# Optimization experiments

Hardware: AMD Instinct MI355X
Metric: run time of the kernel (lower is better)

Reference implementation:

```python
import jax, jax.numpy as jnp
import numpy as np

B, S, D, H = 2, 2048, 1024, 16
DK = D // H  # 64


def setup_inputs() -> dict:
    key = jax.random.key(0)
    ks = jax.random.split(key, 11)
    std = 1.0 / np.sqrt(D)
    inp = {
        "q": jax.random.normal(ks[0], (B, S, D), jnp.float32),
        "k": jax.random.normal(ks[1], (B, S, D), jnp.float32),
        "v": jax.random.normal(ks[2], (B, S, D), jnp.float32),
        # causal mask: True means masked (matches masked_fill(mask == True, -1e9))
        "mask": jnp.triu(jnp.ones((1, 1, S, S), dtype=bool), k=1),
        "Wq": jax.random.normal(ks[3], (D, D), jnp.float32) * std,
        "bq": jnp.zeros((D,), jnp.float32),
        "Wk": jax.random.normal(ks[4], (D, D), jnp.float32) * std,
        "bk": jnp.zeros((D,), jnp.float32),
        "Wv": jax.random.normal(ks[5], (D, D), jnp.float32) * std,
        "bv": jnp.zeros((D,), jnp.float32),
        "Wo": jax.random.normal(ks[6], (D, D), jnp.float32) * std,
        "bo": jnp.zeros((D,), jnp.float32),
    }
    return inp


def _split_heads(x):
    b, s, _ = x.shape
    return x.reshape(b, s, H, DK).transpose(0, 2, 1, 3)  # [B,H,S,DK]


def reference(q, k, v, mask, Wq, bq, Wk, bk, Wv, bv, Wo, bo):
    # QKV projections (nn.Linear: x @ W.T + b)
    qh = _split_heads(q @ Wq.T + bq)
    kh = _split_heads(k @ Wk.T + bk)
    vh = _split_heads(v @ Wv.T + bv)
    # scaled dot-product attention (dropout is identity in eval)
    scores = jnp.einsum("bhqd,bhkd->bhqk", qh, kh) / jnp.sqrt(
        jnp.asarray(DK, jnp.float32))
    scores = jnp.where(mask, jnp.float32(-1e9), scores)
    attn = jax.nn.softmax(scores, axis=-1)
    out = jnp.einsum("bhqk,bhkd->bhqd", attn, vh)
    # combine heads [B,H,S,DK] -> [B,S,D], then output projection
    out = out.transpose(0, 2, 1, 3).reshape(q.shape[0], -1, D)
    return out @ Wo.T + bo
```

## Files before the change

kernel.cpp:

```cpp
#include <hip/hip_runtime.h>
#include <stdint.h>

#define S_LEN 2048
#define DMODEL 1024
#define NHEAD 16
#define DKH 64

typedef __attribute__((ext_vector_type(8))) short short8;
typedef __attribute__((ext_vector_type(4))) short sv4;
typedef __attribute__((ext_vector_type(4))) float fv4;
typedef __attribute__((ext_vector_type(8))) __bf16 bf16x8;
typedef __attribute__((ext_vector_type(4))) float f32x4;

#define QSCALE 0.18033688011112042f

static __device__ __forceinline__ short f2bf(float f) {
  unsigned u = __builtin_bit_cast(unsigned, f);
  u = u + 0x7fffu + ((u >> 16) & 1u);
  return (short)(u >> 16);
}

static __device__ __forceinline__ bf16x8 ldfrag(const void* p) {
  return __builtin_bit_cast(bf16x8, *(const short8*)p);
}

#define GLL16(gp, lp) __builtin_amdgcn_global_load_lds( \
    (const __attribute__((address_space(1))) unsigned int*)(const void*)(gp), \
    (__attribute__((address_space(3))) unsigned int*)(void*)(lp), 16, 0, 0)

#define WAIT_VMCNT(N) asm volatile("s_waitcnt vmcnt(" #N ")" ::: "memory")
#define WAIT_LGKM0()  asm volatile("s_waitcnt lgkmcnt(0)" ::: "memory")

__global__ __launch_bounds__(256) void convert_all(
    const float* __restrict__ q, const float* __restrict__ k, const float* __restrict__ v,
    const float* __restrict__ wq, const float* __restrict__ wk, const float* __restrict__ wv,
    const float* __restrict__ wo,
    short* __restrict__ xb, short* __restrict__ wb, short* __restrict__ wob)
{
  const int total = 4194304;
  for (int gid = blockIdx.x * blockDim.x + threadIdx.x; gid < total;
       gid += gridDim.x * blockDim.x) {
    const float* src; short* dst; int off; float scl = 1.0f;
    if (gid < 3145728) {
      int z = gid >> 20;
      off = (gid & 1048575) << 2;
      src = (z == 0) ? q : (z == 1) ? k : v;
      dst = xb + (size_t)z * 4194304;
    } else {
      int g = gid - 3145728;
      int z = g >> 18;
      off = (g & 262143) << 2;
      src = (z == 0) ? wq : (z == 1) ? wk : (z == 2) ? wv : wo;
      dst = (z < 3) ? (wb + (size_t)z * 1048576) : wob;
      if (z == 0) scl = QSCALE;
    }
    fv4 f = *(const fv4*)(src + off);
    sv4 o;
    o.x = f2bf(f.x * scl); o.y = f2bf(f.y * scl);
    o.z = f2bf(f.z * scl); o.w = f2bf(f.w * scl);
    *(sv4*)(dst + off) = o;
  }
}

__global__ __launch_bounds__(256) void gemm_proj(
    const short* __restrict__ Abase, const short* __restrict__ Wbase,
    const float* __restrict__ bias0, const float* __restrict__ bias1,
    const float* __restrict__ bias2, float bscl0,
    short* __restrict__ Cbf)
{
  const int Kd = 1024, Nd = 1024, Md = 4096;
  const int z = blockIdx.z;
  const short* A = Abase + (size_t)z * Md * Kd;
  const short* W = Wbase + (size_t)z * Nd * Kd;
  const float* bias = (z == 0) ? bias0 : (z == 1) ? bias1 : bias2;
  const float bscl = (z == 0) ? bscl0 : 1.0f;

  __shared__ short8 AB[4096];

  const int tid = threadIdx.x;
  const int w = tid >> 6, lane = tid & 63;
  const int wr = w >> 1, wc = w & 1;
  const int lhi = lane >> 4, llo = lane & 15;
  const int id = blockIdx.x + 8 * blockIdx.y;
  const int sw = (id & 7) * 32 + (id >> 3);
  const int n0 = (sw & 7) * 128, m0 = (sw >> 3) * 128;

  const f32x4 zero = {0.f, 0.f, 0.f, 0.f};
  f32x4 acc[4][4];
#pragma unroll
  for (int i = 0; i < 4; ++i)
#pragma unroll
    for (int j = 0; j < 4; ++j) acc[i][j] = zero;

  auto stage = [&](int buf, int k0) {
#pragma unroll
    for (int inst = 0; inst < 4; ++inst) {
      int ib = w * 4096 + inst * 1024 + lane * 16;
      int row = ib >> 7;
      int colb = (ib & 127) ^ ((row & 7) << 4);
      int col = colb >> 1;
      GLL16(A + (size_t)(m0 + row) * Kd + k0 + col,
            (char*)AB + buf * 32768 + (w * 4096 + inst * 1024));
      GLL16(W + (size_t)(n0 + row) * Kd + k0 + col,
            (char*)AB + buf * 32768 + 16384 + (w * 4096 + inst * 1024));
    }
  };

  stage(0, 0);
  for (int kt = 0; kt < 16; ++kt) {
    const int cur = kt & 1, nxt = cur ^ 1;
    if (kt < 15) {
      stage(nxt, (kt + 1) * 64);
      WAIT_VMCNT(8);
    } else {
      WAIT_VMCNT(0);
    }
    __builtin_amdgcn_s_barrier();
    const char* As = (const char*)AB + cur * 32768;
    const char* Bs = As + 16384;
#pragma unroll
    for (int kk = 0; kk < 2; ++kk) {
      bf16x8 af[4], bfm[4];
#pragma unroll
      for (int t = 0; t < 4; ++t) {
        int arow = wr * 64 + t * 16 + llo;
        int abyte = ((arow << 7) + ((kk * 32 + lhi * 8) << 1)) ^ ((arow & 7) << 4);
        af[t] = ldfrag(As + abyte);
        int brow = wc * 64 + t * 16 + llo;
        int bbyte = ((brow << 7) + ((kk * 32 + lhi * 8) << 1)) ^ ((brow & 7) << 4);
        bfm[t] = ldfrag(Bs + bbyte);
      }
#pragma unroll
      for (int i = 0; i < 4; ++i)
#pragma unroll
        for (int j = 0; j < 4; ++j)
          acc[i][j] = __builtin_amdgcn_mfma_f32_16x16x32_bf16(af[i], bfm[j], acc[i][j], 0, 0, 0);
    }
    __builtin_amdgcn_s_barrier();
  }

  short* Co = Cbf + (size_t)z * Md * Nd;
  __syncthreads();
  short* Cs = (short*)AB;
#pragma unroll
  for (int i = 0; i < 4; ++i) {
#pragma unroll
    for (int j = 0; j < 4; ++j) {
      int col = wc * 64 + j * 16 + llo;
      float bv_ = bias[n0 + col] * bscl;
#pragma unroll
      for (int r = 0; r < 4; ++r) {
        int row = wr * 64 + i * 16 + lhi * 4 + r;
        Cs[row * 128 + col] = f2bf(acc[i][j][r] + bv_);
      }
    }
  }
  __syncthreads();
#pragma unroll
  for (int s = 0; s < 8; ++s) {
    int lb = s * 4096 + tid * 16;
    short8 vL = *(const short8*)((const char*)Cs + lb);
    int row = lb >> 8;
    int colb = lb & 255;
    *(short8*)&Co[(size_t)(m0 + row) * Nd + n0 + (colb >> 1)] = vL;
  }
}

__global__ __launch_bounds__(256) void gemm_out(
    const short* __restrict__ A, const short* __restrict__ W,
    const float* __restrict__ bias, float* __restrict__ Cf)
{
  const int Kd = 1024, Nd = 1024;

  __shared__ short8 AB[3072];

  const int tid = threadIdx.x;
  const int w = tid >> 6, lane = tid & 63;
  const int wr = w >> 1, wc = w & 1;
  const int lhi = lane >> 4, llo = lane & 15;
  const int id = blockIdx.x + 16 * blockIdx.y;
  const int sw = (id & 7) * 64 + (id >> 3);
  const int n0 = (sw & 15) * 64, m0 = (sw >> 4) * 128;

  const f32x4 zero = {0.f, 0.f, 0.f, 0.f};
  f32x4 acc[4][2];
#pragma unroll
  for (int i = 0; i < 4; ++i)
#pragma unroll
    for (int j = 0; j < 2; ++j) acc[i][j] = zero;

  auto stage = [&](int buf, int k0) {
#pragma unroll
    for (int inst = 0; inst < 4; ++inst) {
      int ib = w * 4096 + inst * 1024 + lane * 16;
      int row = ib >> 7;
      int colb = (ib & 127) ^ ((row & 7) << 4);
      GLL16(A + (size_t)(m0 + row) * Kd + k0 + (colb >> 1),
            (char*)AB + buf * 24576 + (w * 4096 + inst * 1024));
    }
#pragma unroll
    for (int inst = 0; inst < 2; ++inst) {
      int ib = w * 2048 + inst * 1024 + lane * 16;
      int row = ib >> 7;
      int colb = (ib & 127) ^ ((row & 7) << 4);
      GLL16(W + (size_t)(n0 + row) * Kd + k0 + (colb >> 1),
            (char*)AB + buf * 24576 + 16384 + (w * 2048 + inst * 1024));
    }
  };

  stage(0, 0);
  for (int kt = 0; kt < 16; ++kt) {
    const int cur = kt & 1, nxt = cur ^ 1;
    if (kt < 15) {
      stage(nxt, (kt + 1) * 64);
      WAIT_VMCNT(6);
    } else {
      WAIT_VMCNT(0);
    }
    __builtin_amdgcn_s_barrier();
    const char* As = (const char*)AB + cur * 24576;
    const char* Bs = As + 16384;
#pragma unroll
    for (int kk = 0; kk < 2; ++kk) {
      bf16x8 af[4], bfm[2];
#pragma unroll
      for (int t = 0; t < 4; ++t) {
        int arow = wr * 64 + t * 16 + llo;
        int abyte = ((arow << 7) + ((kk * 32 + lhi * 8) << 1)) ^ ((arow & 7) << 4);
        af[t] = ldfrag(As + abyte);
      }
#pragma unroll
      for (int j = 0; j < 2; ++j) {
        int brow = wc * 32 + j * 16 + llo;
        int bbyte = ((brow << 7) + ((kk * 32 + lhi * 8) << 1)) ^ ((brow & 7) << 4);
        bfm[j] = ldfrag(Bs + bbyte);
      }
#pragma unroll
      for (int i = 0; i < 4; ++i)
#pragma unroll
        for (int j = 0; j < 2; ++j)
          acc[i][j] = __builtin_amdgcn_mfma_f32_16x16x32_bf16(af[i], bfm[j], acc[i][j], 0, 0, 0);
    }
    __builtin_amdgcn_s_barrier();
  }

#pragma unroll
  for (int i = 0; i < 4; ++i) {
#pragma unroll
    for (int j = 0; j < 2; ++j) {
      int col = n0 + wc * 32 + j * 16 + llo;
      float bv_ = bias[col];
#pragma unroll
      for (int r = 0; r < 4; ++r) {
        int row = m0 + wr * 64 + i * 16 + lhi * 4 + r;
        Cf[(size_t)row * Nd + col] = acc[i][j][r] + bv_;
      }
    }
  }
}

__global__ __launch_bounds__(512) void attn_fwd(
    const short* __restrict__ Qp, const short* __restrict__ Kp,
    const short* __restrict__ Vp, short* __restrict__ Out)
{
  __shared__ short8 Ks[2][512];
  __shared__ short  Vt[64 * 72];
  __shared__ short  PsA[8][16 * 72];

  const int tid = threadIdx.x;
  const int w = tid >> 6, lane = tid & 63;
  const int lhi = lane >> 4, llo = lane & 15;

  const int id = blockIdx.x;
  const int half = id >> 8;
  const int g = id & 255;
  const int bh = g >> 3;
  const int wv = g & 7;
  const int qt = half ? (15 - 2 * wv) : (2 * wv);
  const int nt = 2 * qt + 2;
  const int qbase = qt * 128;
  const int b = bh >> 4, h = bh & 15;
  const size_t rowbase = (size_t)b * S_LEN;
  const short* Kbase = Kp + rowbase * DMODEL + h * DKH;
  const short* Vbase = Vp + rowbase * DMODEL + h * DKH;

  short* Ps = PsA[w];
  const f32x4 zero = {0.f, 0.f, 0.f, 0.f};

  bf16x8 qf[2];
  {
    const short* qrow = Qp + (rowbase + qbase + w * 16 + llo) * DMODEL + h * DKH;
    qf[0] = ldfrag(qrow + lhi * 8);
    qf[1] = ldfrag(qrow + 32 + lhi * 8);
  }

  float mr[4], lr[4];
  f32x4 oacc[4];
#pragma unroll
  for (int r = 0; r < 4; ++r) { mr[r] = -3.0e38f; lr[r] = 0.f; }
#pragma unroll
  for (int dt = 0; dt < 4; ++dt) oacc[dt] = zero;

  const int kvs = lane;

  {
    int ib = tid * 16;
    int row = ib >> 7;
    int colb = (ib & 127) ^ ((row & 7) << 4);
    GLL16(Kbase + (size_t)row * DMODEL + (colb >> 1), (char*)&Ks[0][0] + ib);
  }
  short8 va = *(const short8*)(Vbase + (size_t)kvs * DMODEL + w * 8);

  for (int t = 0; t < nt; ++t) {
    const int cur = t & 1, nxt = cur ^ 1;
    const int kvbase = t * 64;

    asm volatile("s_waitcnt vmcnt(0)" ::: "memory");
#pragma unroll
    for (int j = 0; j < 8; ++j) Vt[(w * 8 + j) * 72 + kvs] = va[j];
    if (t + 1 < nt) {
      const int nb = kvbase + 64;
      int ib = tid * 16;
      int row = ib >> 7;
      int colb = (ib & 127) ^ ((row & 7) << 4);
      GLL16(Kbase + (size_t)(nb + row) * DMODEL + (colb >> 1),
            (char*)&Ks[nxt][0] + ib);
      va = *(const short8*)(Vbase + (size_t)(nb + kvs) * DMODEL + w * 8);
    }
    WAIT_LGKM0();
    __builtin_amdgcn_s_barrier();

    f32x4 sc[4];
#pragma unroll
    for (int tt = 0; tt < 4; ++tt) sc[tt] = zero;
    __builtin_amdgcn_s_setprio(1);
#pragma unroll
    for (int kk = 0; kk < 2; ++kk) {
#pragma unroll
      for (int tt = 0; tt < 4; ++tt) {
        int krow = tt * 16 + llo;
        int kbyte = ((krow << 7) + ((kk * 32 + lhi * 8) << 1)) ^ ((krow & 7) << 4);
        bf16x8 kf = ldfrag((const char*)&Ks[cur][0] + kbyte);
        sc[tt] = __builtin_amdgcn_mfma_f32_16x16x32_bf16(qf[kk], kf, sc[tt], 0, 0, 0);
      }
    }
    __builtin_amdgcn_s_setprio(0);

    const bool diag = (t >= nt - 2);
    float sv[4][4], tmx[4];
#pragma unroll
    for (int r = 0; r < 4; ++r) {
#pragma unroll
      for (int tt = 0; tt < 4; ++tt) {
        float s = sc[tt][r];
        if (diag) {
          int kg = kvbase + tt * 16 + llo;
          int qg = qbase + w * 16 + lhi * 4 + r;
          if (kg > qg) s = -3.0e38f;
        }
        sv[tt][r] = s;
      }
      float trm = fmaxf(fmaxf(sv[0][r], sv[1][r]), fmaxf(sv[2][r], sv[3][r]));
      trm = fmaxf(trm, __shfl_xor(trm, 1));
      trm = fmaxf(trm, __shfl_xor(trm, 2));
      trm = fmaxf(trm, __shfl_xor(trm, 4));
      trm = fmaxf(trm, __shfl_xor(trm, 8));
      tmx[r] = trm;
    }
    bool grow = (tmx[0] > mr[0] + 8.f) || (tmx[1] > mr[1] + 8.f) ||
                (tmx[2] > mr[2] + 8.f) || (tmx[3] > mr[3] + 8.f);
    if (__ballot(grow)) {
#pragma unroll
      for (int r = 0; r < 4; ++r) {
        float mnew = fmaxf(mr[r], tmx[r]);
        float alpha = __builtin_amdgcn_exp2f(mr[r] - mnew);
        mr[r] = mnew;
        lr[r] *= alpha;
#pragma unroll
        for (int dt = 0; dt < 4; ++dt) oacc[dt][r] = oacc[dt][r] * alpha;
      }
    }
#pragma unroll
    for (int r = 0; r < 4; ++r) {
      float rs = 0.f;
#pragma unroll
      for (int tt = 0; tt < 4; ++tt) {
        float pv = __builtin_amdgcn_exp2f(sv[tt][r] - mr[r]);
        rs += pv;
        Ps[(lhi * 4 + r) * 72 + tt * 16 + llo] = f2bf(pv);
      }
      lr[r] += rs;
    }

    __builtin_amdgcn_s_setprio(1);
#pragma unroll
    for (int kk = 0; kk < 2; ++kk) {
      bf16x8 pa = ldfrag(Ps + llo * 72 + kk * 32 + lhi * 8);
#pragma unroll
      for (int dt = 0; dt < 4; ++dt) {
        bf16x8 vf = ldfrag(&Vt[(dt * 16 + llo) * 72 + kk * 32 + lhi * 8]);
        oacc[dt] = __builtin_amdgcn_mfma_f32_16x16x32_bf16(pa, vf, oacc[dt], 0, 0, 0);
      }
    }
    __builtin_amdgcn_s_setprio(0);
    __builtin_amdgcn_s_barrier();
  }

#pragma unroll
  for (int r = 0; r < 4; ++r) {
    float rs = lr[r];
    rs += __shfl_xor(rs, 1);
    rs += __shfl_xor(rs, 2);
    rs += __shfl_xor(rs, 4);
    rs += __shfl_xor(rs, 8);
    lr[r] = rs;
  }
#pragma unroll
  for (int dt = 0; dt < 4; ++dt) {
#pragma unroll
    for (int r = 0; r < 4; ++r) {
      float vv = oacc[dt][r] / lr[r];
      int row = qbase + w * 16 + lhi * 4 + r;
      int col = h * DKH + dt * 16 + llo;
      Out[(rowbase + row) * DMODEL + col] = f2bf(vv);
    }
  }
}

extern "C" void kernel_launch(void* const* d_in, const int* in_sizes, int n_in,
                              void* d_out, int out_size, void* d_ws, size_t ws_size,
                              hipStream_t stream) {
  (void)in_sizes; (void)n_in; (void)out_size; (void)ws_size;
  const float* q  = (const float*)d_in[0];
  const float* k  = (const float*)d_in[1];
  const float* v  = (const float*)d_in[2];
  const float* Wq = (const float*)d_in[4];
  const float* bq = (const float*)d_in[5];
  const float* Wk = (const float*)d_in[6];
  const float* bk = (const float*)d_in[7];
  const float* Wv = (const float*)d_in[8];
  const float* bv = (const float*)d_in[9];
  const float* Wo = (const float*)d_in[10];
  const float* bo = (const float*)d_in[11];
  float* out = (float*)d_out;

  short* xb   = (short*)d_ws;
  short* wb   = xb + 3ull * 4194304;
  short* wob  = wb + 3ull * 1048576;
  short* proj = wob + 1048576;
  short* attno = xb;

  convert_all<<<dim3(2048), dim3(256), 0, stream>>>(q, k, v, Wq, Wk, Wv, Wo, xb, wb, wob);
  gemm_proj<<<dim3(8, 32, 3), dim3(256), 0, stream>>>(xb, wb, bq, bk, bv, QSCALE, proj);
  attn_fwd<<<dim3(512), dim3(512), 0, stream>>>(proj, proj + 4194304ull,
                                                proj + 2ull * 4194304, attno);
  gemm_out<<<dim3(16, 32), dim3(256), 0, stream>>>(attno, wob, bo, out);
}
```

Baseline: 257.3 us.

## Transpose attention MFMAs and keep P in registers with smaller query tiles

The attention kernel now computes S^T and O^T by swapping the MFMA operands, so each lane owns one query row. P probabilities are packed with v_cvt_pk_bf16_f32 and redistributed through lane shuffles instead of a shared-memory round trip, and the per-row max and sum reductions shrink to two cross-lane steps. Query tiles drop from 128 to 64 rows with 256-thread blocks and 1024 blocks, balanced across four causal groupings. This aims to remove LDS traffic and reductions for P and to improve load balance, at the cost of extra shuffles and reloading K/V more often per query row.

```diff
diff --git a/kernel.cpp b/kernel.cpp
--- a/kernel.cpp
+++ b/kernel.cpp
@@ -11,6 +11,8 @@
 typedef __attribute__((ext_vector_type(4))) float fv4;
 typedef __attribute__((ext_vector_type(8))) __bf16 bf16x8;
 typedef __attribute__((ext_vector_type(4))) float f32x4;
+typedef __attribute__((ext_vector_type(2))) unsigned int u32x2;
+typedef __attribute__((ext_vector_type(4))) unsigned int u32x4;
 
 #define QSCALE 0.18033688011112042f
 
@@ -18,6 +20,12 @@
   unsigned u = __builtin_bit_cast(unsigned, f);
   u = u + 0x7fffu + ((u >> 16) & 1u);
   return (short)(u >> 16);
+}
+
+static __device__ __forceinline__ unsigned cvtpk(float a, float b) {
+  unsigned r;
+  asm("v_cvt_pk_bf16_f32 %0, %1, %2" : "=v"(r) : "v"(a), "v"(b));
+  return r;
 }
 
 static __device__ __forceinline__ bf16x8 ldfrag(const void* p) {
@@ -259,32 +267,31 @@
   }
 }
 
-__global__ __launch_bounds__(512) void attn_fwd(
+__global__ __launch_bounds__(256) void attn_fwd(
     const short* __restrict__ Qp, const short* __restrict__ Kp,
     const short* __restrict__ Vp, short* __restrict__ Out)
 {
   __shared__ short8 Ks[2][512];
   __shared__ short  Vt[64 * 72];
-  __shared__ short  PsA[8][16 * 72];
 
   const int tid = threadIdx.x;
   const int w = tid >> 6, lane = tid & 63;
   const int lhi = lane >> 4, llo = lane & 15;
 
   const int id = blockIdx.x;
-  const int half = id >> 8;
-  const int g = id & 255;
+  const int g  = id & 255;
+  const int kq = id >> 8;
+  const int wv = g & 7;
   const int bh = g >> 3;
-  const int wv = g & 7;
-  const int qt = half ? (15 - 2 * wv) : (2 * wv);
-  const int nt = 2 * qt + 2;
-  const int qbase = qt * 128;
+  const int qt = (kq == 0) ? 2 * wv : (kq == 1) ? 31 - 2 * wv
+               : (kq == 2) ? 2 * wv + 1 : 30 - 2 * wv;
+  const int nt = qt + 1;
+  const int qbase = qt * 64;
   const int b = bh >> 4, h = bh & 15;
   const size_t rowbase = (size_t)b * S_LEN;
   const short* Kbase = Kp + rowbase * DMODEL + h * DKH;
   const short* Vbase = Vp + rowbase * DMODEL + h * DKH;
 
-  short* Ps = PsA[w];
   const f32x4 zero = {0.f, 0.f, 0.f, 0.f};
 
   bf16x8 qf[2];
@@ -294,38 +301,50 @@
     qf[1] = ldfrag(qrow + 32 + lhi * 8);
   }
 
-  float mr[4], lr[4];
+  float mr = -3.0e38f, lr = 0.f;
   f32x4 oacc[4];
 #pragma unroll
-  for (int r = 0; r < 4; ++r) { mr[r] = -3.0e38f; lr[r] = 0.f; }
-#pragma unroll
   for (int dt = 0; dt < 4; ++dt) oacc[dt] = zero;
 
-  const int kvs = lane;
-
-  {
-    int ib = tid * 16;
+  const int kvs = lane, dgrp = w;
+
+  const int srcA = (2 * (lhi & 1)) * 16 + llo;
+  const int srcB = srcA + 16;
+  const int t0d = lhi >> 1;
+
+#pragma unroll
+  for (int inst = 0; inst < 2; ++inst) {
+    int ib = w * 2048 + inst * 1024 + lane * 16;
     int row = ib >> 7;
     int colb = (ib & 127) ^ ((row & 7) << 4);
-    GLL16(Kbase + (size_t)row * DMODEL + (colb >> 1), (char*)&Ks[0][0] + ib);
-  }
-  short8 va = *(const short8*)(Vbase + (size_t)kvs * DMODEL + w * 8);
+    GLL16(Kbase + (size_t)row * DMODEL + (colb >> 1),
+          (char*)&Ks[0][0] + (w * 2048 + inst * 1024));
+  }
+  short8 va, vb;
+  va = *(const short8*)(Vbase + (size_t)kvs * DMODEL + dgrp * 16);
+  vb = *(const short8*)(Vbase + (size_t)kvs * DMODEL + dgrp * 16 + 8);
 
   for (int t = 0; t < nt; ++t) {
     const int cur = t & 1, nxt = cur ^ 1;
     const int kvbase = t * 64;
 
-    asm volatile("s_waitcnt vmcnt(0)" ::: "memory");
-#pragma unroll
-    for (int j = 0; j < 8; ++j) Vt[(w * 8 + j) * 72 + kvs] = va[j];
+    WAIT_VMCNT(0);
+#pragma unroll
+    for (int j = 0; j < 8; ++j) Vt[(dgrp * 16 + j) * 72 + kvs] = va[j];
+#pragma unroll
+    for (int j = 0; j < 8; ++j) Vt[(dgrp * 16 + 8 + j) * 72 + kvs] = vb[j];
     if (t + 1 < nt) {
       const int nb = kvbase + 64;
-      int ib = tid * 16;
-      int row = ib >> 7;
-      int colb = (ib & 127) ^ ((row & 7) << 4);
-      GLL16(Kbase + (size_t)(nb + row) * DMODEL + (colb >> 1),
-            (char*)&Ks[nxt][0] + ib);
-      va = *(const short8*)(Vbase + (size_t)(nb + kvs) * DMODEL + w * 8);
+#pragma unroll
+      for (int inst = 0; inst < 2; ++inst) {
+        int ib = w * 2048 + inst * 1024 + lane * 16;
+        int row = ib >> 7;
+        int colb = (ib & 127) ^ ((row & 7) << 4);
+        GLL16(Kbase + (size_t)(nb + row) * DMODEL + (colb >> 1),
+              (char*)&Ks[nxt][0] + (w * 2048 + inst * 1024));
+      }
+      va = *(const short8*)(Vbase + (size_t)(nb + kvs) * DMODEL + dgrp * 16);
+      vb = *(const short8*)(Vbase + (size_t)(nb + kvs) * DMODEL + dgrp * 16 + 8);
     }
     WAIT_LGKM0();
     __builtin_amdgcn_s_barrier();
@@ -341,88 +360,96 @@
         int krow = tt * 16 + llo;
         int kbyte = ((krow << 7) + ((kk * 32 + lhi * 8) << 1)) ^ ((krow & 7) << 4);
         bf16x8 kf = ldfrag((const char*)&Ks[cur][0] + kbyte);
-        sc[tt] = __builtin_amdgcn_mfma_f32_16x16x32_bf16(qf[kk], kf, sc[tt], 0, 0, 0);
+        sc[tt] = __builtin_amdgcn_mfma_f32_16x16x32_bf16(kf, qf[kk], sc[tt], 0, 0, 0);
       }
     }
     __builtin_amdgcn_s_setprio(0);
 
-    const bool diag = (t >= nt - 2);
-    float sv[4][4], tmx[4];
-#pragma unroll
-    for (int r = 0; r < 4; ++r) {
-#pragma unroll
-      for (int tt = 0; tt < 4; ++tt) {
+    const bool diag = (t == qt);
+    float sv[4][4];
+#pragma unroll
+    for (int tt = 0; tt < 4; ++tt) {
+#pragma unroll
+      for (int r = 0; r < 4; ++r) {
         float s = sc[tt][r];
         if (diag) {
-          int kg = kvbase + tt * 16 + llo;
-          int qg = qbase + w * 16 + lhi * 4 + r;
+          int kg = kvbase + tt * 16 + lhi * 4 + r;
+          int qg = qbase + w * 16 + llo;
           if (kg > qg) s = -3.0e38f;
         }
         sv[tt][r] = s;
       }
-      float trm = fmaxf(fmaxf(sv[0][r], sv[1][r]), fmaxf(sv[2][r], sv[3][r]));
-      trm = fmaxf(trm, __shfl_xor(trm, 1));
-      trm = fmaxf(trm, __shfl_xor(trm, 2));
-      trm = fmaxf(trm, __shfl_xor(trm, 4));
-      trm = fmaxf(trm, __shfl_xor(trm, 8));
-      tmx[r] = trm;
-    }
-    bool grow = (tmx[0] > mr[0] + 8.f) || (tmx[1] > mr[1] + 8.f) ||
-                (tmx[2] > mr[2] + 8.f) || (tmx[3] > mr[3] + 8.f);
-    if (__ballot(grow)) {
+    }
+    float pmax = -3.0e38f;
+#pragma unroll
+    for (int tt = 0; tt < 4; ++tt)
+      pmax = fmaxf(pmax, fmaxf(fmaxf(sv[tt][0], sv[tt][1]),
+                               fmaxf(sv[tt][2], sv[tt][3])));
+    pmax = fmaxf(pmax, __shfl_xor(pmax, 16));
+    pmax = fmaxf(pmax, __shfl_xor(pmax, 32));
+
+    if (__ballot(pmax > mr + 8.f)) {
+      float mnew = fmaxf(mr, pmax);
+      float alpha = __builtin_amdgcn_exp2f(mr - mnew);
+      mr = mnew;
+      lr *= alpha;
+#pragma unroll
+      for (int dt = 0; dt < 4; ++dt) oacc[dt] = oacc[dt] * alpha;
+    }
+
+    float p[4][4];
+#pragma unroll
+    for (int tt = 0; tt < 4; ++tt)
 #pragma unroll
       for (int r = 0; r < 4; ++r) {
-        float mnew = fmaxf(mr[r], tmx[r]);
-        float alpha = __builtin_amdgcn_exp2f(mr[r] - mnew);
-        mr[r] = mnew;
-        lr[r] *= alpha;
-#pragma unroll
-        for (int dt = 0; dt < 4; ++dt) oacc[dt][r] = oacc[dt][r] * alpha;
-      }
-    }
-#pragma unroll
-    for (int r = 0; r < 4; ++r) {
-      float rs = 0.f;
-#pragma unroll
-      for (int tt = 0; tt < 4; ++tt) {
-        float pv = __builtin_amdgcn_exp2f(sv[tt][r] - mr[r]);
-        rs += pv;
-        Ps[(lhi * 4 + r) * 72 + tt * 16 + llo] = f2bf(pv);
-      }
-      lr[r] += rs;
+        p[tt][r] = __builtin_amdgcn_exp2f(sv[tt][r] - mr);
+        lr += p[tt][r];
+      }
+    unsigned plo[4], phi[4];
+#pragma unroll
+    for (int tt = 0; tt < 4; ++tt) {
+      plo[tt] = cvtpk(p[tt][0], p[tt][1]);
+      phi[tt] = cvtpk(p[tt][2], p[tt][3]);
     }
 
     __builtin_amdgcn_s_setprio(1);
 #pragma unroll
     for (int kk = 0; kk < 2; ++kk) {
-      bf16x8 pa = ldfrag(Ps + llo * 72 + kk * 32 + lhi * 8);
+      unsigned aL0 = __shfl((int)plo[2 * kk + 0], srcA);
+      unsigned aH0 = __shfl((int)phi[2 * kk + 0], srcA);
+      unsigned aL1 = __shfl((int)plo[2 * kk + 1], srcA);
+      unsigned aH1 = __shfl((int)phi[2 * kk + 1], srcA);
+      unsigned bL0 = __shfl((int)plo[2 * kk + 0], srcB);
+      unsigned bH0 = __shfl((int)phi[2 * kk + 0], srcB);
+      unsigned bL1 = __shfl((int)plo[2 * kk + 1], srcB);
+      unsigned bH1 = __shfl((int)phi[2 * kk + 1], srcB);
+      u32x4 pw;
+      pw.x = t0d ? aL1 : aL0;
+      pw.y = t0d ? aH1 : aH0;
+      pw.z = t0d ? bL1 : bL0;
+      pw.w = t0d ? bH1 : bH0;
+      bf16x8 pb = __builtin_bit_cast(bf16x8, pw);
 #pragma unroll
       for (int dt = 0; dt < 4; ++dt) {
         bf16x8 vf = ldfrag(&Vt[(dt * 16 + llo) * 72 + kk * 32 + lhi * 8]);
-        oacc[dt] = __builtin_amdgcn_mfma_f32_16x16x32_bf16(pa, vf, oacc[dt], 0, 0, 0);
+        oacc[dt] = __builtin_amdgcn_mfma_f32_16x16x32_bf16(vf, pb, oacc[dt], 0, 0, 0);
       }
     }
     __builtin_amdgcn_s_setprio(0);
     __builtin_amdgcn_s_barrier();
   }
 
-#pragma unroll
-  for (int r = 0; r < 4; ++r) {
-    float rs = lr[r];
-    rs += __shfl_xor(rs, 1);
-    rs += __shfl_xor(rs, 2);
-    rs += __shfl_xor(rs, 4);
-    rs += __shfl_xor(rs, 8);
-    lr[r] = rs;
-  }
-#pragma unroll
-  for (int dt = 0; dt < 4; ++dt) {
-#pragma unroll
-    for (int r = 0; r < 4; ++r) {
-      float vv = oacc[dt][r] / lr[r];
-      int row = qbase + w * 16 + lhi * 4 + r;
-      int col = h * DKH + dt * 16 + llo;
-      Out[(rowbase + row) * DMODEL + col] = f2bf(vv);
+  lr += __shfl_xor(lr, 16);
+  lr += __shfl_xor(lr, 32);
+  float inv = 1.0f / lr;
+  {
+    short* orow = Out + (rowbase + qbase + w * 16 + llo) * DMODEL + h * DKH;
+#pragma unroll
+    for (int dt = 0; dt < 4; ++dt) {
+      u32x2 st;
+      st.x = cvtpk(oacc[dt][0] * inv, oacc[dt][1] * inv);
+      st.y = cvtpk(oacc[dt][2] * inv, oacc[dt][3] * inv);
+      *(u32x2*)&orow[dt * 16 + lhi * 4] = st;
     }
   }
 }
@@ -452,7 +479,7 @@
 
   convert_all<<<dim3(2048), dim3(256), 0, stream>>>(q, k, v, Wq, Wk, Wv, Wo, xb, wb, wob);
   gemm_proj<<<dim3(8, 32, 3), dim3(256), 0, stream>>>(xb, wb, bq, bk, bv, QSCALE, proj);
-  attn_fwd<<<dim3(512), dim3(512), 0, stream>>>(proj, proj + 4194304ull,
-                                                proj + 2ull * 4194304, attno);
+  attn_fwd<<<dim3(1024), dim3(256), 0, stream>>>(proj, proj + 4194304ull,
+                                                 proj + 2ull * 4194304, attno);
   gemm_out<<<dim3(16, 32), dim3(256), 0, stream>>>(attno, wob, bo, out);
 }
```

Result: faster. 238.5 us (-7.3%).
